# Performance work log

Measured on AMD Instinct MI355X. Metric: run time of the kernel, lower is better.

## Reference

```python
import jax, jax.numpy as jnp
import numpy as np


def setup_inputs() -> dict:
    key = jax.random.key(0)
    k1, k2, k3, k4 = jax.random.split(key, 4)
    B, S, H = 32768, 128, 64
    origins = jax.random.normal(k1, (B, 3), dtype=jnp.float32)
    directions = jax.random.normal(k2, (B, 3), dtype=jnp.float32)
    W1 = jax.random.normal(k3, (3, H), dtype=jnp.float32) * 0.5
    b1 = jnp.zeros((H,), dtype=jnp.float32)
    W2 = jax.random.normal(k4, (H, 4), dtype=jnp.float32) * 0.1
    b2 = jnp.zeros((4,), dtype=jnp.float32)
    return {
        "origins": origins,
        "directions": directions,
        "near": jnp.float32(2.0),
        "far": jnp.float32(6.0),
        "W1": W1,
        "b1": b1,
        "W2": W2,
        "b2": b2,
        "num_samples": S,
    }


def reference(origins, directions, near, far, W1, b1, W2, b2, num_samples):
    B = origins.shape[0]
    S = num_samples
    # segment boundaries [S+1] and midpoints [S] along each ray
    t = jnp.linspace(0.0, 1.0, S + 1, dtype=origins.dtype)
    boundaries = near + (far - near) * t                      # [S+1]
    mids = 0.5 * (boundaries[1:] + boundaries[:-1])           # [S]
    # normalized directions (F.normalize with eps clamp on norm)
    norm = jnp.linalg.norm(directions, axis=-1, keepdims=True)
    d = directions / jnp.maximum(norm, 1e-12)                 # [B,3]
    # sample locations [B,S,3]
    samples = origins[:, None, :] + mids[None, :, None] * d[:, None, :]
    # field: 2-layer ReLU MLP, exp-mapped outputs
    x = samples.reshape(-1, 3)                                # [B*S,3]
    h = jax.nn.relu(x @ W1 + b1)                              # [B*S,H]
    field_values = jnp.exp(h @ W2 + b2)                       # [B*S,4]
    sigmas = field_values[:, -1].reshape(B, S)                # [B,S]
    colors = field_values[:, :-1].reshape(B, S, 3)            # [B,S,3]
    # alpha values from densities and segment lengths
    deltas = boundaries[1:] - boundaries[:-1]                 # [S]
    alphas = 1.0 - jnp.exp(-sigmas * deltas[None, :])         # [B,S]
    # alpha compositing (inclusive cumprod, as in the source)
    T = jnp.cumprod(1.0 - alphas, axis=-1)                    # [B,S]
    w = T * alphas                                            # [B,S]
    return jnp.einsum("bs,bsc->bc", w, colors)                # [B,3]
```

## Files before the change

### kernel.cpp

```cpp
#include <hip/hip_runtime.h>


constexpr int S_TOTAL = 128;
constexpr int TPR     = 16;
constexpr int SPT     = S_TOTAL / TPR;
constexpr int BLOCK   = 256;
constexpr int RPB     = BLOCK / TPR;
constexpr int H       = 64;

__global__ __launch_bounds__(BLOCK, 8)
void nerf_fused(const float* __restrict__ origins,
                const float* __restrict__ directions,
                const float* __restrict__ nearp,
                const float* __restrict__ farp,
                const float* __restrict__ W1,
                const float* __restrict__ b1,
                const float* __restrict__ W2,
                const float* __restrict__ b2,
                float* __restrict__ out,
                int B)
{
    __shared__ float ABs[RPB][H + 1][2];
    __shared__ float W2s[H][4];
    __shared__ float b2s[4];

    const int tid  = threadIdx.x;
    const int ray0 = blockIdx.x * RPB;

    if (tid < H) {
        W2s[tid][0] = W2[tid * 4 + 0];
        W2s[tid][1] = W2[tid * 4 + 1];
        W2s[tid][2] = W2[tid * 4 + 2];
        W2s[tid][3] = W2[tid * 4 + 3];
    }
    if (tid < 4) b2s[tid] = b2[tid];

#pragma unroll
    for (int idx = tid; idx < RPB * H; idx += BLOCK) {
        const int r   = idx >> 6;
        const int h   = idx & (H - 1);
        const int ray = ray0 + r;
        const float o0 = origins[ray * 3 + 0];
        const float o1 = origins[ray * 3 + 1];
        const float o2 = origins[ray * 3 + 2];
        float d0 = directions[ray * 3 + 0];
        float d1 = directions[ray * 3 + 1];
        float d2 = directions[ray * 3 + 2];
        const float nrm  = sqrtf(d0 * d0 + d1 * d1 + d2 * d2);
        const float rinv = 1.0f / fmaxf(nrm, 1e-12f);
        d0 *= rinv; d1 *= rinv; d2 *= rinv;
        const float w0 = W1[0 * H + h];
        const float w1 = W1[1 * H + h];
        const float w2 = W1[2 * H + h];
        ABs[r][h][0] = fmaf(o2, w2, fmaf(o1, w1, fmaf(o0, w0, b1[h])));
        ABs[r][h][1] = fmaf(d2, w2, fmaf(d1, w1, d0 * w0));
    }
    __syncthreads();

    const int sub  = tid & (TPR - 1);
    const int rloc = tid >> 4;
    const int ray  = ray0 + rloc;

    const float nr    = nearp[0];
    const float fr    = farp[0];
    const float delta = (fr - nr) * (1.0f / (float)S_TOTAL);

    float m[SPT];
#pragma unroll
    for (int k = 0; k < SPT; ++k)
        m[k] = fmaf((float)(sub * SPT + k) + 0.5f, delta, nr);

    const float b20 = b2s[0], b21 = b2s[1], b22 = b2s[2], b23 = b2s[3];
    float4 acc[SPT];
#pragma unroll
    for (int k = 0; k < SPT; ++k) acc[k] = make_float4(b20, b21, b22, b23);

#pragma unroll 4
    for (int h = 0; h < H; ++h) {
        const float2 ab = *reinterpret_cast<const float2*>(&ABs[rloc][h][0]);
        const float4 pb = *reinterpret_cast<const float4*>(&W2s[h][0]);
#pragma unroll
        for (int k = 0; k < SPT; ++k) {
            const float hv = fmaxf(fmaf(m[k], ab.y, ab.x), 0.0f);
            acc[k].x = fmaf(hv, pb.x, acc[k].x);
            acc[k].y = fmaf(hv, pb.y, acc[k].y);
            acc[k].z = fmaf(hv, pb.z, acc[k].z);
            acc[k].w = fmaf(hv, pb.w, acc[k].w);
        }
    }

    float Tloc = 1.0f, orr = 0.0f, og = 0.0f, ob = 0.0f;
#pragma unroll
    for (int k = 0; k < SPT; ++k) {
        const float sig = __expf(acc[k].w);
        const float e   = __expf(-sig * delta);
        Tloc *= e;
        const float w = Tloc * (1.0f - e);
        orr = fmaf(w, __expf(acc[k].x), orr);
        og  = fmaf(w, __expf(acc[k].y), og);
        ob  = fmaf(w, __expf(acc[k].z), ob);
    }

    float scan = Tloc;
#pragma unroll
    for (int off = 1; off < TPR; off <<= 1) {
        const float v = __shfl_up(scan, off, TPR);
        if (sub >= off) scan *= v;
    }
    float pre = __shfl_up(scan, 1, TPR);
    if (sub == 0) pre = 1.0f;

    orr *= pre; og *= pre; ob *= pre;
#pragma unroll
    for (int off = TPR / 2; off > 0; off >>= 1) {
        orr += __shfl_down(orr, off, TPR);
        og  += __shfl_down(og,  off, TPR);
        ob  += __shfl_down(ob,  off, TPR);
    }

    if (sub == 0) {
        out[ray * 3 + 0] = orr;
        out[ray * 3 + 1] = og;
        out[ray * 3 + 2] = ob;
    }
}

extern "C" void kernel_launch(void* const* d_in, const int* in_sizes, int n_in,
                              void* d_out, int out_size, void* d_ws, size_t ws_size,
                              hipStream_t stream) {
    const float* origins    = (const float*)d_in[0];
    const float* directions = (const float*)d_in[1];
    const float* nearp      = (const float*)d_in[2];
    const float* farp       = (const float*)d_in[3];
    const float* W1         = (const float*)d_in[4];
    const float* b1         = (const float*)d_in[5];
    const float* W2         = (const float*)d_in[6];
    const float* b2         = (const float*)d_in[7];
    float* out              = (float*)d_out;

    const int B     = in_sizes[0] / 3;
    const int total = B * TPR;
    const int grid  = (total + BLOCK - 1) / BLOCK;

    nerf_fused<<<grid, BLOCK, 0, stream>>>(origins, directions, nearp, farp,
                                           W1, b1, W2, b2, out, B);
}
```

Baseline: 40.69 us.

## Exploit piecewise-linear ReLU over sample intervals to skip per-sample MLP work

Each thread's samples lie on one line segment, so hidden unit h = A + m*B. A unit whose ReLU state is the same at both ends of the thread's interval contributes a linear term, which is folded into per-thread P/Q accumulators. Only units that switch sign inside the interval get the full per-sample correction. This removes most of the per-sample FMA work but adds divergent branches within a wavefront. It also lowers the launch-bounds occupancy hint from 8 to 4 and computes midpoints by running addition, which changes rounding slightly.

Measured after the change: 41.53 us. +2.1%, slower.

```diff
diff --git a/kernel.cpp b/kernel.cpp
--- a/kernel.cpp
+++ b/kernel.cpp
@@ -1,5 +1,7 @@
 #include <hip/hip_runtime.h>
 
+
+typedef float v2f __attribute__((ext_vector_type(2)));
 
 constexpr int S_TOTAL = 128;
 constexpr int TPR     = 16;
@@ -8,30 +10,28 @@
 constexpr int RPB     = BLOCK / TPR;
 constexpr int H       = 64;
 
-__global__ __launch_bounds__(BLOCK, 8)
-void nerf_fused(const float* __restrict__ origins,
-                const float* __restrict__ directions,
-                const float* __restrict__ nearp,
-                const float* __restrict__ farp,
-                const float* __restrict__ W1,
-                const float* __restrict__ b1,
-                const float* __restrict__ W2,
-                const float* __restrict__ b2,
-                float* __restrict__ out,
-                int B)
+__global__ __launch_bounds__(BLOCK, 4)
+void nerf_ival(const float* __restrict__ origins,
+               const float* __restrict__ directions,
+               const float* __restrict__ nearp,
+               const float* __restrict__ farp,
+               const float* __restrict__ W1,
+               const float* __restrict__ b1,
+               const float* __restrict__ W2,
+               const float* __restrict__ b2,
+               float* __restrict__ out,
+               int B)
 {
-    __shared__ float ABs[RPB][H + 1][2];
-    __shared__ float W2s[H][4];
+    __shared__ v2f ABs2[RPB][H + 1];
+    __shared__ v2f W2p[H][2];
     __shared__ float b2s[4];
 
     const int tid  = threadIdx.x;
     const int ray0 = blockIdx.x * RPB;
 
     if (tid < H) {
-        W2s[tid][0] = W2[tid * 4 + 0];
-        W2s[tid][1] = W2[tid * 4 + 1];
-        W2s[tid][2] = W2[tid * 4 + 2];
-        W2s[tid][3] = W2[tid * 4 + 3];
+        W2p[tid][0] = (v2f){W2[tid * 4 + 0], W2[tid * 4 + 1]};
+        W2p[tid][1] = (v2f){W2[tid * 4 + 2], W2[tid * 4 + 3]};
     }
     if (tid < 4) b2s[tid] = b2[tid];
 
@@ -49,11 +49,12 @@
         const float nrm  = sqrtf(d0 * d0 + d1 * d1 + d2 * d2);
         const float rinv = 1.0f / fmaxf(nrm, 1e-12f);
         d0 *= rinv; d1 *= rinv; d2 *= rinv;
-        const float w0 = W1[0 * H + h];
-        const float w1 = W1[1 * H + h];
-        const float w2 = W1[2 * H + h];
-        ABs[r][h][0] = fmaf(o2, w2, fmaf(o1, w1, fmaf(o0, w0, b1[h])));
-        ABs[r][h][1] = fmaf(d2, w2, fmaf(d1, w1, d0 * w0));
+        const float u0 = W1[0 * H + h];
+        const float u1 = W1[1 * H + h];
+        const float u2 = W1[2 * H + h];
+        const float A  = fmaf(o2, u2, fmaf(o1, u1, fmaf(o0, u0, b1[h])));
+        const float Bc = fmaf(d2, u2, fmaf(d1, u1, d0 * u0));
+        ABs2[r][h] = (v2f){A, Bc};
     }
     __syncthreads();
 
@@ -66,39 +67,64 @@
     const float delta = (fr - nr) * (1.0f / (float)S_TOTAL);
 
     float m[SPT];
+    m[0] = fmaf((float)(sub * SPT) + 0.5f, delta, nr);
 #pragma unroll
-    for (int k = 0; k < SPT; ++k)
-        m[k] = fmaf((float)(sub * SPT + k) + 0.5f, delta, nr);
+    for (int k = 1; k < SPT; ++k) m[k] = m[k - 1] + delta;
+    const float m0 = m[0], m7 = m[SPT - 1];
 
-    const float b20 = b2s[0], b21 = b2s[1], b22 = b2s[2], b23 = b2s[3];
-    float4 acc[SPT];
+    float acc[4][SPT];
 #pragma unroll
-    for (int k = 0; k < SPT; ++k) acc[k] = make_float4(b20, b21, b22, b23);
+    for (int k = 0; k < SPT; ++k) {
+        acc[0][k] = b2s[0]; acc[1][k] = b2s[1];
+        acc[2][k] = b2s[2]; acc[3][k] = b2s[3];
+    }
+
+    float P0 = 0.f, P1 = 0.f, P2 = 0.f, P3 = 0.f;
+    float Q0 = 0.f, Q1 = 0.f, Q2 = 0.f, Q3 = 0.f;
 
 #pragma unroll 4
     for (int h = 0; h < H; ++h) {
-        const float2 ab = *reinterpret_cast<const float2*>(&ABs[rloc][h][0]);
-        const float4 pb = *reinterpret_cast<const float4*>(&W2s[h][0]);
+        const v2f ab  = ABs2[rloc][h];
+        const v2f w01 = W2p[h][0];
+        const v2f w23 = W2p[h][1];
+        const float g0 = fmaf(m0, ab.y, ab.x);
+        const float g7 = fmaf(m7, ab.y, ab.x);
+        const bool act0 = g0 > 0.0f;
+        const bool act7 = g7 > 0.0f;
+        const float Am = act0 ? ab.x : 0.0f;
+        const float Bm = act0 ? ab.y : 0.0f;
+        P0 = fmaf(w01.x, Am, P0); P1 = fmaf(w01.y, Am, P1);
+        P2 = fmaf(w23.x, Am, P2); P3 = fmaf(w23.y, Am, P3);
+        Q0 = fmaf(w01.x, Bm, Q0); Q1 = fmaf(w01.y, Bm, Q1);
+        Q2 = fmaf(w23.x, Bm, Q2); Q3 = fmaf(w23.y, Bm, Q3);
+        if (act0 != act7) {
 #pragma unroll
-        for (int k = 0; k < SPT; ++k) {
-            const float hv = fmaxf(fmaf(m[k], ab.y, ab.x), 0.0f);
-            acc[k].x = fmaf(hv, pb.x, acc[k].x);
-            acc[k].y = fmaf(hv, pb.y, acc[k].y);
-            acc[k].z = fmaf(hv, pb.z, acc[k].z);
-            acc[k].w = fmaf(hv, pb.w, acc[k].w);
+            for (int k = 0; k < SPT; ++k) {
+                const float gk  = fmaf(m[k], ab.y, ab.x);
+                const float sel = act0 ? gk : 0.0f;
+                const float ck  = fmaxf(gk, 0.0f) - sel;
+                acc[0][k] = fmaf(ck, w01.x, acc[0][k]);
+                acc[1][k] = fmaf(ck, w01.y, acc[1][k]);
+                acc[2][k] = fmaf(ck, w23.x, acc[2][k]);
+                acc[3][k] = fmaf(ck, w23.y, acc[3][k]);
+            }
         }
     }
 
     float Tloc = 1.0f, orr = 0.0f, og = 0.0f, ob = 0.0f;
 #pragma unroll
     for (int k = 0; k < SPT; ++k) {
-        const float sig = __expf(acc[k].w);
+        const float c0 = fmaf(m[k], Q0, P0) + acc[0][k];
+        const float c1 = fmaf(m[k], Q1, P1) + acc[1][k];
+        const float c2 = fmaf(m[k], Q2, P2) + acc[2][k];
+        const float sg = fmaf(m[k], Q3, P3) + acc[3][k];
+        const float sig = __expf(sg);
         const float e   = __expf(-sig * delta);
         Tloc *= e;
         const float w = Tloc * (1.0f - e);
-        orr = fmaf(w, __expf(acc[k].x), orr);
-        og  = fmaf(w, __expf(acc[k].y), og);
-        ob  = fmaf(w, __expf(acc[k].z), ob);
+        orr = fmaf(w, __expf(c0), orr);
+        og  = fmaf(w, __expf(c1), og);
+        ob  = fmaf(w, __expf(c2), ob);
     }
 
     float scan = Tloc;
@@ -142,6 +168,6 @@
     const int total = B * TPR;
     const int grid  = (total + BLOCK - 1) / BLOCK;
 
-    nerf_fused<<<grid, BLOCK, 0, stream>>>(origins, directions, nearp, farp,
-                                           W1, b1, W2, b2, out, B);
+    nerf_ival<<<grid, BLOCK, 0, stream>>>(origins, directions, nearp, farp,
+                                          W1, b1, W2, b2, out, B);
 }
```
